# Optimization experiments

Measured on AMD Instinct MI355X. Metric: run time of the kernel, lower is better.

The kernel has to match this reference:

```python
import jax, jax.numpy as jnp
import numpy as np

# dims per init_kwargs / input_specs
B, C, H, W = 8, 256, 56, 56
K = 3            # kernel_size
S = 1            # stride
D = 1            # dilation
HEAD = 1
MID = int(C * 0.2)   # se_ratio bottleneck = 51
GAIN = float(np.sqrt(2.0))  # calculate_gain('relu')


def setup_inputs() -> dict:
    key = jax.random.key(0)
    ks = jax.random.split(key, 6)
    sc = 0.05
    return {
        "x": jax.random.normal(ks[0], (B, C, H, W), jnp.float32),
        # channel branch: 1x1 convs stored as dense matrices
        "w1": jax.random.normal(ks[1], (MID, C), jnp.float32) * sc,
        "b1": jnp.zeros((MID,), jnp.float32),
        "w2": jax.random.normal(ks[2], (C * K * K, MID), jnp.float32) * sc,
        "b2": jnp.zeros((C * K * K,), jnp.float32),
        # spatial branch: 1x1 conv c -> head*k^2
        "ws": jax.random.normal(ks[3], (HEAD * K * K, C), jnp.float32) * sc,
        "bs": jnp.zeros((HEAD * K * K,), jnp.float32),
        # FilterNorm running_std parameter (channel branch): randn * gain/k
        "fn_std": jax.random.normal(ks[4], (C * K * K,), jnp.float32) * (GAIN / K),
    }


def _ddf_mul(x, cf, sf):
    """Decoupled dynamic filter, 'mul' combine.
    x: (B,C,H,W), cf: (B,C,K,K) channel filter, sf: (B,K*K,Ho,Wo) spatial filter.
    out[b,c,i,j] = sum_{u,v} x[b,c, i*S+(u-(K-1)/2)*D, j*S+(v-(K-1)/2)*D] * cf[b,c,u,v] * sf[b,u*K+v,i,j]
    Accumulate over the K*K taps to avoid materializing the unfolded tensor."""
    p = D * (K - 1) // 2
    xp = jnp.pad(x, ((0, 0), (0, 0), (p, p), (p, p)))
    Ho, Wo = H // S, W // S
    out = jnp.zeros((B, C, Ho, Wo), x.dtype)
    for u in range(K):
        for v in range(K):
            patch = xp[:, :, u * D:u * D + S * Ho:S, v * D:v * D + S * Wo:S]
            out = out + patch * cf[:, :, u, v][:, :, None, None] * sf[:, u * K + v][:, None]
    return out


def reference(x, w1, b1, w2, b2, ws, bs, fn_std):
    # ---- channel branch: SE-style filter generation ----
    pooled = x.mean((2, 3))                                  # (B,C) global avg pool
    y = jax.nn.relu(pooled @ w1.T + b1)                      # (B,MID)
    y = (y @ w2.T + b2).reshape(B, C, K * K)                 # (B,C,K^2)
    # FilterNorm 'channel': normalize over K^2 (torch std -> ddof=1), learned std
    y = (y - y.mean(-1, keepdims=True)) / (y.std(-1, ddof=1, keepdims=True) + 1e-10)
    cf = (y.reshape(B, C * K * K) * fn_std).reshape(B, C, K, K)
    # ---- spatial branch: 1x1 conv (stride S) + FilterNorm 'spatial' ----
    xs = x[:, :, ::S, ::S]
    sf = jnp.einsum('bchw,nc->bnhw', xs, ws) + bs[None, :, None, None]  # (B,K^2,Ho,Wo)
    sf = sf.reshape(B, HEAD, K * K, H // S, W // S)
    sf = (sf - sf.mean(2, keepdims=True)) / (sf.std(2, ddof=1, keepdims=True) + 1e-10)
    sf = sf.reshape(B, HEAD * K * K, H // S, W // S) * (GAIN / K)
    # ---- fused per-pixel gather-multiply-reduce (head=1 -> no group reshape) ----
    return _ddf_mul(x, cf, sf)
```

## Files before the change

### kernel.cpp

```cpp
#include <hip/hip_runtime.h>
#include <math.h>

#define BB   8
#define CC   256
#define HH   56
#define WW   56
#define KK   3
#define MIDN 51
#define NTAP (KK*KK)
#define CKK  (CC*NTAP)
#define HW   (HH*WW)
#define NCH  8
#define CPC  (CC/NCH)
#define PBLK 13
#define NCPB 2

__global__ __launch_bounds__(256) void k_sfpool(const float* __restrict__ x,
                                                const float* __restrict__ ws,
                                                float* __restrict__ partial,
                                                float* __restrict__ poolpart) {
    int blk = blockIdx.x;
    int pb = blk % PBLK;
    int tmp = blk / PBLK;
    int chunk = tmp % NCH;
    int b = tmp / NCH;
    int t = threadIdx.x;
    int wave = t >> 6, lane = t & 63;
    __shared__ float wss[NTAP][CPC];
    __shared__ float wsum[4][CPC];
    for (int idx = t; idx < NTAP * CPC; idx += 256) {
        int n = idx / CPC, c = idx - n * CPC;
        wss[n][c] = ws[n * CC + chunk * CPC + c];
    }
    __syncthreads();
    int p = pb * 256 + t;
    bool act = (p < HW);
    float acc[NTAP];
    #pragma unroll
    for (int n = 0; n < NTAP; ++n) acc[n] = 0.f;
    const float* xp = x + ((size_t)(b * CC + chunk * CPC)) * HW + p;
    for (int c = 0; c < CPC; ++c) {
        float xv = act ? xp[(size_t)c * HW] : 0.f;
        #pragma unroll
        for (int n = 0; n < NTAP; ++n) acc[n] += xv * wss[n][c];
        float s = xv;
        s += __shfl_down(s, 32, 64);
        s += __shfl_down(s, 16, 64);
        s += __shfl_down(s, 8, 64);
        s += __shfl_down(s, 4, 64);
        s += __shfl_down(s, 2, 64);
        s += __shfl_down(s, 1, 64);
        if (lane == 0) wsum[wave][c] = s;
    }
    __syncthreads();
    if (t < CPC) {
        float psum = wsum[0][t] + wsum[1][t] + wsum[2][t] + wsum[3][t];
        poolpart[((size_t)((b * NCH + chunk) * PBLK + pb)) * CPC + t] = psum;
    }
    if (act) {
        float* pp = partial + ((size_t)((b * NCH + chunk) * NTAP)) * HW + p;
        #pragma unroll
        for (int n = 0; n < NTAP; ++n) pp[(size_t)n * HW] = acc[n];
    }
}

#define MLPBLK (BB*NCH)
#define W2CHUNK (CPC*NTAP*MIDN)
__global__ __launch_bounds__(256) void k_mlp_sfB(const float* __restrict__ poolpart,
                                                 const float* __restrict__ w1,
                                                 const float* __restrict__ b1,
                                                 const float* __restrict__ w2,
                                                 const float* __restrict__ b2,
                                                 const float* __restrict__ fn_std,
                                                 const float* __restrict__ partial,
                                                 const float* __restrict__ bs,
                                                 float* __restrict__ cf,
                                                 float* __restrict__ sf) {
    __shared__ float smem[W2CHUNK + 256 + 64 + CPC * NTAP];
    float* w2s = smem;
    float* ps  = smem + W2CHUNK;
    float* y1  = ps + 256;
    float* y2s = y1 + 64;
    int blk = blockIdx.x;
    int t = threadIdx.x;
    if (blk < MLPBLK) {
        int b = blk >> 3, chunk = blk & 7;
        int c0 = chunk * CPC;
        const float4* w2v = (const float4*)(w2 + (size_t)chunk * W2CHUNK);
        float4* w2s4 = (float4*)w2s;
        for (int i = t; i < W2CHUNK / 4; i += 256) w2s4[i] = w2v[i];
        {
            int chunkp = t >> 5, cl = t & 31;
            float s = 0.f;
            const float* pp = poolpart + ((size_t)(b * NCH + chunkp) * PBLK) * CPC + cl;
            #pragma unroll
            for (int pb = 0; pb < PBLK; ++pb) s += pp[pb * CPC];
            ps[t] = s * (1.0f / HW);
        }
        __syncthreads();
        if (t < MIDN) {
            float acc = b1[t];
            const float* wr = w1 + t * CC;
            for (int c2 = 0; c2 < CC; ++c2) acc += ps[c2] * wr[c2];
            y1[t] = fmaxf(acc, 0.f);
        }
        __syncthreads();
        #pragma unroll
        for (int base = 0; base < 512; base += 256) {
            int idx = base + t;
            if (idx < CPC * NTAP) {
                float acc = b2[c0 * NTAP + idx];
                const float* r = w2s + idx * MIDN;
                #pragma unroll 3
                for (int m = 0; m < MIDN; ++m) acc += y1[m] * r[m];
                y2s[idx] = acc;
            }
        }
        __syncthreads();
        if (t < CPC) {
            int c = c0 + t;
            float y2[NTAP];
            #pragma unroll
            for (int q = 0; q < NTAP; ++q) y2[q] = y2s[t * NTAP + q];
            float mean = 0.f;
            #pragma unroll
            for (int q = 0; q < NTAP; ++q) mean += y2[q];
            mean *= (1.f / NTAP);
            float var = 0.f;
            #pragma unroll
            for (int q = 0; q < NTAP; ++q) { float d = y2[q] - mean; var += d * d; }
            float inv = 1.f / (sqrtf(var * (1.f / (NTAP - 1))) + 1e-10f);
            #pragma unroll
            for (int q = 0; q < NTAP; ++q) {
                int idx = c * NTAP + q;
                cf[(size_t)b * CKK + idx] = (y2[q] - mean) * inv * fn_std[idx];
            }
        }
    } else {
        int sblk = blk - MLPBLK;
        int b = sblk / PBLK, pb = sblk % PBLK;
        int p = pb * 256 + t;
        if (p >= HW) return;
        float acc[NTAP];
        #pragma unroll
        for (int n = 0; n < NTAP; ++n) acc[n] = bs[n];
        const float* pp = partial + ((size_t)(b * NCH)) * NTAP * HW + p;
        for (int chunk = 0; chunk < NCH; ++chunk)
            #pragma unroll
            for (int n = 0; n < NTAP; ++n)
                acc[n] += pp[((size_t)(chunk * NTAP + n)) * HW];
        float mean = 0.f;
        #pragma unroll
        for (int n = 0; n < NTAP; ++n) mean += acc[n];
        mean *= (1.f / NTAP);
        float var = 0.f;
        #pragma unroll
        for (int n = 0; n < NTAP; ++n) { float d = acc[n] - mean; var += d * d; }
        float inv = 0.47140452079103173f /
                    (sqrtf(var * (1.f / (NTAP - 1))) + 1e-10f);
        #pragma unroll
        for (int n = 0; n < NTAP; ++n)
            sf[((size_t)(b * NTAP + n)) * HW + p] = (acc[n] - mean) * inv;
    }
}

__global__ __launch_bounds__(256) void k_ddf(const float* __restrict__ x,
                                             const float* __restrict__ cf,
                                             const float* __restrict__ sf,
                                             float* __restrict__ out) {
    int blk = blockIdx.x;
    int b = blk / (CC / NCPB), cg = blk % (CC / NCPB);
    int c0 = cg * NCPB;
    int t = threadIdx.x;
    __shared__ float xt[NCPB][58 * 58];
    for (int idx = t; idx < NCPB * 58 * 58; idx += 256) ((float*)xt)[idx] = 0.f;
    __syncthreads();
    const float* xp = x + ((size_t)(b * CC + c0)) * HW;
    for (int idx = t; idx < HW; idx += 256) {
        int r = idx / WW, col = idx - r * WW;
        int o = (r + 1) * 58 + col + 1;
        xt[0][o] = xp[idx];
        xt[1][o] = xp[HW + idx];
    }
    float cf9[NCPB][NTAP];
    const float* cfp = cf + (size_t)b * CKK + c0 * NTAP;
    #pragma unroll
    for (int k = 0; k < NCPB; ++k)
        #pragma unroll
        for (int n = 0; n < NTAP; ++n) cf9[k][n] = cfp[k * NTAP + n];
    __syncthreads();
    const float* sfb = sf + (size_t)b * NTAP * HW;
    float* op = out + ((size_t)(b * CC + c0)) * HW;
    for (int idx = t; idx < HW; idx += 256) {
        int i = idx / WW, j = idx - i * WW;
        float s9[NTAP];
        #pragma unroll
        for (int n = 0; n < NTAP; ++n) s9[n] = sfb[(size_t)n * HW + idx];
        float acc0 = 0.f, acc1 = 0.f;
        #pragma unroll
        for (int u = 0; u < KK; ++u)
            #pragma unroll
            for (int v = 0; v < KK; ++v) {
                int n = u * KK + v;
                int o = (i + u) * 58 + (j + v);
                float xv0 = xt[0][o], xv1 = xt[1][o];
                acc0 += xv0 * (cf9[0][n] * s9[n]);
                acc1 += xv1 * (cf9[1][n] * s9[n]);
            }
        op[idx] = acc0;
        op[HW + idx] = acc1;
    }
}

extern "C" void kernel_launch(void* const* d_in, const int* in_sizes, int n_in,
                              void* d_out, int out_size, void* d_ws, size_t ws_size,
                              hipStream_t stream) {
    const float* x      = (const float*)d_in[0];
    const float* w1     = (const float*)d_in[1];
    const float* b1     = (const float*)d_in[2];
    const float* w2     = (const float*)d_in[3];
    const float* b2     = (const float*)d_in[4];
    const float* ws     = (const float*)d_in[5];
    const float* bs     = (const float*)d_in[6];
    const float* fn_std = (const float*)d_in[7];
    float* out = (float*)d_out;

    float* wsf      = (float*)d_ws;
    float* cf       = wsf;
    float* sf       = cf + 18432;
    float* poolpart = sf + 225792;
    float* partial  = poolpart + 26624;

    k_sfpool<<<BB * NCH * PBLK, 256, 0, stream>>>(x, ws, partial, poolpart);
    k_mlp_sfB<<<MLPBLK + BB * PBLK, 256, 0, stream>>>(poolpart, w1, b1, w2, b2,
                                                      fn_std, partial, bs, cf, sf);
    k_ddf<<<BB * (CC / NCPB), 256, 0, stream>>>(x, cf, sf, out);
}
```

Before: 132.9 us.

## Process four channels per DDF block with float4 loads; halve sfpool channel chunks

The DDF kernel now handles four channels per block instead of two, so each spatial-filter value read from global memory is reused across more channels. The input tile is loaded with float4 global reads. The sfpool stage uses four channel chunks instead of eight, and the MLP kernel is adjusted to keep its own 32-channel partition while reading the new pooled layout. The cost is about 54KB of shared memory per DDF block, which lowers occupancy, and half as many DDF blocks.

Result: slower. 143.5 us (+8.0%).

```diff
diff --git a/kernel.cpp b/kernel.cpp
--- a/kernel.cpp
+++ b/kernel.cpp
@@ -10,10 +10,11 @@
 #define NTAP (KK*KK)
 #define CKK  (CC*NTAP)
 #define HW   (HH*WW)
-#define NCH  8
+#define NCH  4
 #define CPC  (CC/NCH)
 #define PBLK 13
-#define NCPB 2
+#define NCPB 4
+#define TILE 3364
 
 __global__ __launch_bounds__(256) void k_sfpool(const float* __restrict__ x,
                                                 const float* __restrict__ ws,
@@ -64,8 +65,8 @@
     }
 }
 
-#define MLPBLK (BB*NCH)
-#define W2CHUNK (CPC*NTAP*MIDN)
+#define MLPBLK (BB*8)
+#define W2CHUNK (32*NTAP*MIDN)
 __global__ __launch_bounds__(256) void k_mlp_sfB(const float* __restrict__ poolpart,
                                                  const float* __restrict__ w1,
                                                  const float* __restrict__ b1,
@@ -76,7 +77,7 @@
                                                  const float* __restrict__ bs,
                                                  float* __restrict__ cf,
                                                  float* __restrict__ sf) {
-    __shared__ float smem[W2CHUNK + 256 + 64 + CPC * NTAP];
+    __shared__ float smem[W2CHUNK + 256 + 64 + 32 * NTAP];
     float* w2s = smem;
     float* ps  = smem + W2CHUNK;
     float* y1  = ps + 256;
@@ -84,13 +85,13 @@
     int blk = blockIdx.x;
     int t = threadIdx.x;
     if (blk < MLPBLK) {
-        int b = blk >> 3, chunk = blk & 7;
-        int c0 = chunk * CPC;
-        const float4* w2v = (const float4*)(w2 + (size_t)chunk * W2CHUNK);
+        int b = blk >> 3, mchunk = blk & 7;
+        int c0 = mchunk * 32;
+        const float4* w2v = (const float4*)(w2 + (size_t)mchunk * W2CHUNK);
         float4* w2s4 = (float4*)w2s;
         for (int i = t; i < W2CHUNK / 4; i += 256) w2s4[i] = w2v[i];
         {
-            int chunkp = t >> 5, cl = t & 31;
+            int chunkp = t >> 6, cl = t & 63;
             float s = 0.f;
             const float* pp = poolpart + ((size_t)(b * NCH + chunkp) * PBLK) * CPC + cl;
             #pragma unroll
@@ -108,7 +109,7 @@
         #pragma unroll
         for (int base = 0; base < 512; base += 256) {
             int idx = base + t;
-            if (idx < CPC * NTAP) {
+            if (idx < 32 * NTAP) {
                 float acc = b2[c0 * NTAP + idx];
                 const float* r = w2s + idx * MIDN;
                 #pragma unroll 3
@@ -117,7 +118,7 @@
             }
         }
         __syncthreads();
-        if (t < CPC) {
+        if (t < 32) {
             int c = c0 + t;
             float y2[NTAP];
             #pragma unroll
@@ -172,15 +173,18 @@
     int b = blk / (CC / NCPB), cg = blk % (CC / NCPB);
     int c0 = cg * NCPB;
     int t = threadIdx.x;
-    __shared__ float xt[NCPB][58 * 58];
-    for (int idx = t; idx < NCPB * 58 * 58; idx += 256) ((float*)xt)[idx] = 0.f;
-    __syncthreads();
-    const float* xp = x + ((size_t)(b * CC + c0)) * HW;
-    for (int idx = t; idx < HW; idx += 256) {
-        int r = idx / WW, col = idx - r * WW;
-        int o = (r + 1) * 58 + col + 1;
-        xt[0][o] = xp[idx];
-        xt[1][o] = xp[HW + idx];
+    __shared__ float xt[NCPB][TILE];
+    for (int idx = t; idx < NCPB * TILE; idx += 256) ((float*)xt)[idx] = 0.f;
+    __syncthreads();
+    const float4* xp4 = (const float4*)(x + ((size_t)(b * CC + c0)) * HW);
+    for (int i4 = t; i4 < NCPB * HW / 4; i4 += 256) {
+        float4 v = xp4[i4];
+        int k = i4 / (HW / 4);
+        int rem4 = i4 - k * (HW / 4);
+        int r = rem4 / (WW / 4);
+        int col = 4 * (rem4 - r * (WW / 4));
+        float* d = &xt[k][(r + 1) * 58 + col + 1];
+        d[0] = v.x; d[1] = v.y; d[2] = v.z; d[3] = v.w;
     }
     float cf9[NCPB][NTAP];
     const float* cfp = cf + (size_t)b * CKK + c0 * NTAP;
@@ -196,19 +200,21 @@
         float s9[NTAP];
         #pragma unroll
         for (int n = 0; n < NTAP; ++n) s9[n] = sfb[(size_t)n * HW + idx];
-        float acc0 = 0.f, acc1 = 0.f;
+        float acc[NCPB];
+        #pragma unroll
+        for (int k = 0; k < NCPB; ++k) acc[k] = 0.f;
         #pragma unroll
         for (int u = 0; u < KK; ++u)
             #pragma unroll
             for (int v = 0; v < KK; ++v) {
                 int n = u * KK + v;
                 int o = (i + u) * 58 + (j + v);
-                float xv0 = xt[0][o], xv1 = xt[1][o];
-                acc0 += xv0 * (cf9[0][n] * s9[n]);
-                acc1 += xv1 * (cf9[1][n] * s9[n]);
+                #pragma unroll
+                for (int k = 0; k < NCPB; ++k)
+                    acc[k] += xt[k][o] * (cf9[k][n] * s9[n]);
             }
-        op[idx] = acc0;
-        op[HW + idx] = acc1;
+        #pragma unroll
+        for (int k = 0; k < NCPB; ++k) op[(size_t)k * HW + idx] = acc[k];
     }
 }
 
```
